# Optimization experiments

Measured on AMD Instinct MI355X. Metric: run time of the kernel, lower is better.

The kernel has to match this reference:

```python
import jax, jax.numpy as jnp
import numpy as np

SEQ_LEN = 2048
NUM_HEADS = 16
DIM_EMB = 1024
DIM_HEAD = DIM_EMB // NUM_HEADS  # 64
DIM_K = DIM_EMB  # source scales by dim_k**-0.5 with dim_k defaulting to dim_emb
BASE = 10000
EPS = float(np.finfo(np.float32).eps)


def _rope_tables(seq_len, dim_head):
    idx = jnp.arange(seq_len, dtype=jnp.float32)
    scale = 1.0 / (BASE ** (jnp.arange(0, dim_head, 2, dtype=jnp.float32) / dim_head) + EPS)
    pos = jnp.outer(idx, scale)              # [S, dh/2]
    pos = jnp.concatenate([pos, pos], axis=-1)  # [S, dh]
    return jnp.cos(pos), jnp.sin(pos)


def _rotate_half(x):
    x1, x2 = x[..., : DIM_HEAD // 2], x[..., DIM_HEAD // 2 :]
    return jnp.concatenate([-x2, x1], axis=-1)


def _apply_rope(x, cos, sin):
    # x: [B, H, S, dh]; cos/sin: [S, dh]
    return x * cos[None, None] + _rotate_half(x) * sin[None, None]


def setup_inputs() -> dict:
    key = jax.random.key(0)
    k1, k2, k3 = jax.random.split(key, 3)
    x = jax.random.normal(k1, (2, SEQ_LEN, DIM_EMB), dtype=jnp.float32)
    Wqkv = jax.random.normal(k2, (DIM_EMB, 3 * DIM_EMB), dtype=jnp.float32) * 0.02
    Wout = jax.random.normal(k3, (DIM_EMB, DIM_EMB), dtype=jnp.float32) * 0.02
    return {"x": x, "Wqkv": Wqkv, "Wout": Wout}


def reference(x, Wqkv, Wout):
    B = x.shape[0]
    cos, sin = _rope_tables(SEQ_LEN, DIM_HEAD)
    qkv = x @ Wqkv  # [B, S, 3*E]
    q, k, v = jnp.split(qkv, 3, axis=-1)

    def to_heads(t):
        return t.reshape(B, SEQ_LEN, NUM_HEADS, DIM_HEAD).transpose(0, 2, 1, 3)

    q, k, v = to_heads(q), to_heads(k), to_heads(v)
    q = _apply_rope(q, cos, sin)
    k = _apply_rope(k, cos, sin)

    scores = jnp.einsum('bhsd,bhtd->bhst', q, k) * (DIM_K ** -0.5)
    causal_mask = jnp.triu(jnp.ones((SEQ_LEN, SEQ_LEN), dtype=bool), k=1)
    scores = jnp.where(causal_mask[None, None], -jnp.inf, scores)
    attn = jax.nn.softmax(scores, axis=-1)
    out = jnp.einsum('bhst,bhtd->bhsd', attn, v)
    out = out.transpose(0, 2, 1, 3).reshape(B, SEQ_LEN, DIM_EMB)
    return out @ Wout
```

## Files before the change

kernel.cpp:

```cpp
#include <hip/hip_runtime.h>

#define S_LEN 2048
#define NHEAD 16

using f32x4  = __attribute__((ext_vector_type(4))) float;
using f32x16 = __attribute__((ext_vector_type(16))) float;
using bf16x8 = __attribute__((ext_vector_type(8))) __bf16;

__device__ __forceinline__ unsigned short f2bf(float f) {
  union { float f; unsigned u; } v; v.f = f;
  unsigned r = v.u + 0x7FFFu + ((v.u >> 16) & 1u);
  return (unsigned short)(r >> 16);
}
__device__ __forceinline__ float bf2f(unsigned short h) {
  union { unsigned u; float f; } v; v.u = ((unsigned)h) << 16; return v.f;
}
__device__ __forceinline__ void unpack8(uint4 u, float x[8]) {
  x[0]=bf2f((unsigned short)(u.x&0xffff)); x[1]=bf2f((unsigned short)(u.x>>16));
  x[2]=bf2f((unsigned short)(u.y&0xffff)); x[3]=bf2f((unsigned short)(u.y>>16));
  x[4]=bf2f((unsigned short)(u.z&0xffff)); x[5]=bf2f((unsigned short)(u.z>>16));
  x[6]=bf2f((unsigned short)(u.w&0xffff)); x[7]=bf2f((unsigned short)(u.w>>16));
}
__device__ __forceinline__ uint4 pack8(const unsigned short o[8]) {
  uint4 u;
  u.x = (unsigned)o[0] | ((unsigned)o[1]<<16);
  u.y = (unsigned)o[2] | ((unsigned)o[3]<<16);
  u.z = (unsigned)o[4] | ((unsigned)o[5]<<16);
  u.w = (unsigned)o[6] | ((unsigned)o[7]<<16);
  return u;
}
__device__ __forceinline__ void gload16(const void* g, void* l) {
  __builtin_amdgcn_global_load_lds(
      (const __attribute__((address_space(1))) unsigned int*)g,
      (__attribute__((address_space(3))) unsigned int*)l, 16, 0, 0);
}
__device__ __forceinline__ float exp2_fast(float x) {
#if __has_builtin(__builtin_amdgcn_exp2f)
  return __builtin_amdgcn_exp2f(x);
#else
  return __expf(x * 0.6931471805599453f);
#endif
}
__device__ __forceinline__ void store_c(float* C, size_t off, float v) { C[off] = v; }
__device__ __forceinline__ void store_c(unsigned short* C, size_t off, float v) { C[off] = f2bf(v); }

__global__ __launch_bounds__(256) void k_cvt(const float* __restrict__ in,
                                             unsigned short* __restrict__ out, int n8) {
  int i = blockIdx.x * 256 + threadIdx.x;
  if (i >= n8) return;
  const float4* p = (const float4*)in + 2 * (size_t)i;
  float4 a = p[0], b = p[1];
  unsigned short o[8] = { f2bf(a.x), f2bf(a.y), f2bf(a.z), f2bf(a.w),
                          f2bf(b.x), f2bf(b.y), f2bf(b.z), f2bf(b.w) };
  ((uint4*)out)[i] = pack8(o);
}

__global__ __launch_bounds__(256) void k_transpose_cvt(const float* __restrict__ in,
                                                       unsigned short* __restrict__ out,
                                                       int R, int C) {
  __shared__ float T[64][65];
  int r0 = blockIdx.x * 64, c0 = blockIdx.y * 64;
  int tid = threadIdx.x;
#pragma unroll
  for (int i = 0; i < 16; ++i) {
    int idx = tid + i * 256;
    int r = idx >> 6, c = idx & 63;
    T[r][c] = in[(size_t)(r0 + r) * C + c0 + c];
  }
  __syncthreads();
#pragma unroll
  for (int i = 0; i < 8; ++i) {
    int idx = tid + i * 256;
    int co = idx >> 5, rp = (idx & 31) * 2;
    unsigned v = (unsigned)f2bf(T[rp][co]) | ((unsigned)f2bf(T[rp + 1][co]) << 16);
    *(unsigned*)&out[(size_t)(c0 + co) * R + r0 + rp] = v;
  }
}

template <typename OUT_T>
__global__ __launch_bounds__(256, 2) void k_gemm128(const unsigned short* __restrict__ A,
                                                    const unsigned short* __restrict__ Bt,
                                                    OUT_T* __restrict__ C,
                                                    int M, int N, int K) {
  __shared__ unsigned short As[2][128][64];
  __shared__ unsigned short Bs[2][128][64];
  const int tid = threadIdx.x;
  const int lane = tid & 63, w = tid >> 6;
  const int wm = w >> 1, wn = w & 1;
  const int li = lane & 15, g = lane >> 4;
  const int m0 = blockIdx.x * 128, n0 = blockIdx.y * 128;
  const int srow = w * 8 + (lane >> 3);
  const int scol = ((lane & 7) ^ ((lane >> 3) & 7)) * 8;

  f32x4 acc[4][4];
#pragma unroll
  for (int i = 0; i < 4; ++i)
#pragma unroll
    for (int j = 0; j < 4; ++j) acc[i][j] = (f32x4){0.f, 0.f, 0.f, 0.f};

  const int nt = K >> 6;

  auto stage_tile = [&](int kt) {
    int buf = kt & 1;
    const unsigned short* sa = A + (size_t)(m0 + srow) * K + kt * 64 + scol;
    const unsigned short* sb = Bt + (size_t)(n0 + srow) * K + kt * 64 + scol;
    char* da = (char*)&As[buf][srow][0];
    char* db = (char*)&Bs[buf][srow][0];
#pragma unroll
    for (int j = 0; j < 4; ++j) {
      gload16(sa + (size_t)(j * 32) * K, da + j * 32 * 128);
      gload16(sb + (size_t)(j * 32) * K, db + j * 32 * 128);
    }
  };

  stage_tile(0);

  for (int i = 0; i < nt; ++i) {
    if (i + 1 < nt) {
      stage_tile(i + 1);
      asm volatile("s_waitcnt vmcnt(8)" ::: "memory");
    } else {
      asm volatile("s_waitcnt vmcnt(0)" ::: "memory");
    }
    __builtin_amdgcn_s_barrier();
    asm volatile("" ::: "memory");
    const int buf = i & 1;
#pragma unroll
    for (int kk = 0; kk < 2; ++kk) {
      bf16x8 af[4], bfv[4];
      const int ps = ((kk << 2) | g) ^ (li & 7);
#pragma unroll
      for (int ii = 0; ii < 4; ++ii)
        af[ii] = *(const bf16x8*)&As[buf][wm * 64 + ii * 16 + li][ps * 8];
#pragma unroll
      for (int jj = 0; jj < 4; ++jj)
        bfv[jj] = *(const bf16x8*)&Bs[buf][wn * 64 + jj * 16 + li][ps * 8];
      __builtin_amdgcn_s_setprio(1);
#pragma unroll
      for (int ii = 0; ii < 4; ++ii)
#pragma unroll
        for (int jj = 0; jj < 4; ++jj)
          acc[ii][jj] = __builtin_amdgcn_mfma_f32_16x16x32_bf16(af[ii], bfv[jj],
                                                                acc[ii][jj], 0, 0, 0);
      __builtin_amdgcn_s_setprio(0);
    }
    asm volatile("" ::: "memory");
    __builtin_amdgcn_s_barrier();
    asm volatile("" ::: "memory");
  }

#pragma unroll
  for (int ii = 0; ii < 4; ++ii) {
    int row = m0 + wm * 64 + ii * 16 + g * 4;
#pragma unroll
    for (int jj = 0; jj < 4; ++jj) {
      int col = n0 + wn * 64 + jj * 16 + li;
#pragma unroll
      for (int r = 0; r < 4; ++r) store_c(C, (size_t)(row + r) * N + col, acc[ii][jj][r]);
    }
  }
}

__global__ __launch_bounds__(256) void k_rope_split(const unsigned short* __restrict__ qkv,
                                                    unsigned short* __restrict__ Qf,
                                                    unsigned short* __restrict__ Kf,
                                                    unsigned short* __restrict__ Vf) {
  int blk = blockIdx.x;
  int st = blk & 31, h = (blk >> 5) & 15, b = blk >> 9;
  int s0 = st * 64;
  int tid = threadIdx.x;
  int sl = tid >> 2, quad = tid & 3;
  int s = s0 + sl;
  int bh = b * NHEAD + h;
  int l31 = s & 31;
  int qt = s >> 5;
  int cq = quad >> 1, hiq = quad & 1;

  float cs[8], sn[8];
#pragma unroll
  for (int j = 0; j < 8; ++j) {
    int pr = quad * 8 + j;
    float e2 = exp2_fast((float)pr * 0.41524101f);
    float freq = 1.0f / (e2 + 1.1920928955078125e-07f);
    float x = (float)s * freq * 0.15915494309189535f;
    x -= floorf(x);
    float ang = x * 6.283185307179586f;
    sn[j] = __sinf(ang);
    cs[j] = __cosf(ang);
  }
  const unsigned short* row = qkv + (size_t)(b * S_LEN + s) * 3072;
  const float QSC = 0.04508422f;
  {
    float x1[8], x2[8];
    unpack8(*(const uint4*)&row[h * 64 + quad * 8], x1);
    unpack8(*(const uint4*)&row[h * 64 + 32 + quad * 8], x2);
    unsigned short o1[8], o2[8];
#pragma unroll
    for (int j = 0; j < 8; ++j) {
      o1[j] = f2bf((x1[j] * cs[j] - x2[j] * sn[j]) * QSC);
      o2[j] = f2bf((x2[j] * cs[j] + x1[j] * sn[j]) * QSC);
    }
    size_t base = ((size_t)bh * 64 + qt) * 4;
    int lane8 = (hiq * 32 + l31) * 8;
    *(uint4*)&Qf[(base + cq) * 512 + lane8] = pack8(o1);
    *(uint4*)&Qf[(base + 2 + cq) * 512 + lane8] = pack8(o2);
  }
  {
    float x1[8], x2[8];
    unpack8(*(const uint4*)&row[1024 + h * 64 + quad * 8], x1);
    unpack8(*(const uint4*)&row[1024 + h * 64 + 32 + quad * 8], x2);
    unsigned short o1[8], o2[8];
#pragma unroll
    for (int j = 0; j < 8; ++j) {
      o1[j] = f2bf(x1[j] * cs[j] - x2[j] * sn[j]);
      o2[j] = f2bf(x2[j] * cs[j] + x1[j] * sn[j]);
    }
    int lp = (l31 & 0x13) | ((l31 & 4) << 1) | ((l31 & 8) >> 1);
    size_t base = ((size_t)bh * 64 + qt) * 4;
    int lane8 = (hiq * 32 + lp) * 8;
    *(uint4*)&Kf[(base + cq) * 512 + lane8] = pack8(o1);
    *(uint4*)&Kf[(base + 2 + cq) * 512 + lane8] = pack8(o2);
  }
  __shared__ unsigned short Vl[64 * 72];
#pragma unroll
  for (int i = 0; i < 2; ++i) {
    int c = tid + i * 256;
    int r = c >> 3, c8 = (c & 7) * 8;
    *(uint4*)&Vl[r * 72 + c8] =
        *(const uint4*)&qkv[(size_t)(b * S_LEN + s0 + r) * 3072 + 2048 + h * 64 + c8];
  }
  __syncthreads();
  int d = tid >> 2, sc4 = tid & 3;
  unsigned o[8];
#pragma unroll
  for (int jj = 0; jj < 8; ++jj) {
    int sidx = sc4 * 16 + jj * 2;
    o[jj] = (unsigned)Vl[sidx * 72 + d] | ((unsigned)Vl[(sidx + 1) * 72 + d] << 16);
  }
  {
    int t = st * 2 + (sc4 >> 1);
    int c = ((d >> 5) << 1) + (sc4 & 1);
    size_t base = (((size_t)bh * 64 + t) * 4 + c) * 512;
    *(uint4*)&Vf[base + (d & 31) * 8]        = make_uint4(o[0], o[1], o[2], o[3]);
    *(uint4*)&Vf[base + (32 + (d & 31)) * 8] = make_uint4(o[4], o[5], o[6], o[7]);
  }
}

__global__ __launch_bounds__(256) void k_attn5(const unsigned short* __restrict__ Qf,
                                               const unsigned short* __restrict__ Kf,
                                               const unsigned short* __restrict__ Vf,
                                               unsigned short* __restrict__ O) {
  __shared__ float MBUF[3][2176];
  int bid = blockIdx.x;
  int i = (bid & 7) * 256 + (bid >> 3);
  int bh = i >> 6;
  int qt = 63 - (i & 63);
  int tid = threadIdx.x, w = tid >> 6, lane = tid & 63;
  int b = bh >> 4, h = bh & 15;
  int l31 = lane & 31, hi = lane >> 5;

  int n = qt + 1;
  int t0 = (w * n) >> 2, t1 = ((w + 1) * n) >> 2;

  const unsigned short* Kg = Kf + ((size_t)bh * 64) * 4 * 512 + lane * 8;
  const unsigned short* Vg = Vf + ((size_t)bh * 64) * 4 * 512 + lane * 8;

  float m_run = -1e30f, l_run = 0.f;
  f32x16 acc0, acc1;
#pragma unroll
  for (int r = 0; r < 16; ++r) { acc0[r] = 0.f; acc1[r] = 0.f; }

  if (t0 < t1) {
    const unsigned short* Qg = Qf + (((size_t)bh * 64 + qt) * 4) * 512 + lane * 8;
    bf16x8 qf[4];
#pragma unroll
    for (int c = 0; c < 4; ++c) qf[c] = *(const bf16x8*)(Qg + c * 512);

    auto loadK = [&](bf16x8 (&kf)[4], int t) {
      const unsigned short* kp = Kg + (size_t)t * 2048;
#pragma unroll
      for (int c = 0; c < 4; ++c) kf[c] = *(const bf16x8*)(kp + c * 512);
    };
    auto loadV = [&](bf16x8 (&vf)[4], int t) {
      const unsigned short* vp = Vg + (size_t)t * 2048;
#pragma unroll
      for (int c = 0; c < 4; ++c) vf[c] = *(const bf16x8*)(vp + c * 512);
    };
    auto rescale_check = [&](float pmax) {
      if (__any(pmax > m_run + 8.0f)) {
        float pfull = fmaxf(pmax, __shfl_xor(pmax, 32));
        float mnew = fmaxf(m_run, pfull);
        float fac = exp2_fast(m_run - mnew);
        l_run *= fac;
#pragma unroll
        for (int r = 0; r < 16; ++r) { acc0[r] *= fac; acc1[r] *= fac; }
        m_run = mnew;
      }
    };
    auto cvt2 = [&](const f32x16& s, bf16x8& p0, bf16x8& p1) {
      unsigned w0, w1, w2, w3;
      asm("v_cvt_pk_bf16_f32 %0, %1, %2" : "=v"(w0) : "v"(s[0]), "v"(s[1]));
      asm("v_cvt_pk_bf16_f32 %0, %1, %2" : "=v"(w1) : "v"(s[2]), "v"(s[3]));
      asm("v_cvt_pk_bf16_f32 %0, %1, %2" : "=v"(w2) : "v"(s[4]), "v"(s[5]));
      asm("v_cvt_pk_bf16_f32 %0, %1, %2" : "=v"(w3) : "v"(s[6]), "v"(s[7]));
      union { uint4 uu; bf16x8 v; } cv;
      cv.uu = make_uint4(w0, w1, w2, w3);
      p0 = cv.v;
      asm("v_cvt_pk_bf16_f32 %0, %1, %2" : "=v"(w0) : "v"(s[8]), "v"(s[9]));
      asm("v_cvt_pk_bf16_f32 %0, %1, %2" : "=v"(w1) : "v"(s[10]), "v"(s[11]));
      asm("v_cvt_pk_bf16_f32 %0, %1, %2" : "=v"(w2) : "v"(s[12]), "v"(s[13]));
      asm("v_cvt_pk_bf16_f32 %0, %1, %2" : "=v"(w3) : "v"(s[14]), "v"(s[15]));
      cv.uu = make_uint4(w0, w1, w2, w3);
      p1 = cv.v;
    };

    bf16x8 kA[4], vA[4], kB[4], vB[4];
    loadK(kA, t0); loadV(vA, t0);
    if (t0 + 1 < t1) { loadK(kB, t0 + 1); loadV(vB, t0 + 1); }
    int t = t0;
    while (t + 1 < t1) {
      int tb = t + 1;
      f32x16 sa, sb;
#pragma unroll
      for (int r = 0; r < 16; ++r) { sa[r] = 0.f; sb[r] = 0.f; }
      __builtin_amdgcn_s_setprio(1);
      sa = __builtin_amdgcn_mfma_f32_32x32x16_bf16(kA[0], qf[0], sa, 0, 0, 0);
      sb = __builtin_amdgcn_mfma_f32_32x32x16_bf16(kB[0], qf[0], sb, 0, 0, 0);
      sa = __builtin_amdgcn_mfma_f32_32x32x16_bf16(kA[1], qf[1], sa, 0, 0, 0);
      sb = __builtin_amdgcn_mfma_f32_32x32x16_bf16(kB[1], qf[1], sb, 0, 0, 0);
      sa = __builtin_amdgcn_mfma_f32_32x32x16_bf16(kA[2], qf[2], sa, 0, 0, 0);
      sb = __builtin_amdgcn_mfma_f32_32x32x16_bf16(kB[2], qf[2], sb, 0, 0, 0);
      sa = __builtin_amdgcn_mfma_f32_32x32x16_bf16(kA[3], qf[3], sa, 0, 0, 0);
      sb = __builtin_amdgcn_mfma_f32_32x32x16_bf16(kB[3], qf[3], sb, 0, 0, 0);
      __builtin_amdgcn_s_setprio(0);
      if (t + 2 < t1) loadK(kA, t + 2);
      if (t + 3 < t1) loadK(kB, t + 3);
      if (tb == qt) {
#pragma unroll
        for (int r = 0; r < 16; ++r) {
          int kv = (r & 7) + 16 * (r >> 3) + 8 * hi;
          if (kv > l31) sb[r] = -1e30f;
        }
      }
      float pmax;
      {
        float m[8];
#pragma unroll
        for (int r = 0; r < 8; ++r)
          m[r] = fmaxf(fmaxf(sa[2 * r], sa[2 * r + 1]), fmaxf(sb[2 * r], sb[2 * r + 1]));
        m[0] = fmaxf(m[0], m[1]); m[2] = fmaxf(m[2], m[3]);
        m[4] = fmaxf(m[4], m[5]); m[6] = fmaxf(m[6], m[7]);
        pmax = fmaxf(fmaxf(m[0], m[2]), fmaxf(m[4], m[6]));
      }
      rescale_check(pmax);
#pragma unroll
      for (int r = 0; r < 16; ++r) {
        sa[r] = exp2_fast(sa[r] - m_run);
        sb[r] = exp2_fast(sb[r] - m_run);
      }
      {
        float t0_ = 0.f, t1_ = 0.f, t2_ = 0.f, t3_ = 0.f;
#pragma unroll
        for (int r = 0; r < 4; ++r) {
          t0_ += sa[r] + sb[r];
          t1_ += sa[4 + r] + sb[4 + r];
          t2_ += sa[8 + r] + sb[8 + r];
          t3_ += sa[12 + r] + sb[12 + r];
        }
        l_run += (t0_ + t1_) + (t2_ + t3_);
      }
      bf16x8 pa0, pa1, pb0, pb1;
      cvt2(sa, pa0, pa1);
      cvt2(sb, pb0, pb1);
      __builtin_amdgcn_s_setprio(1);
      acc0 = __builtin_amdgcn_mfma_f32_32x32x16_bf16(vA[0], pa0, acc0, 0, 0, 0);
      acc1 = __builtin_amdgcn_mfma_f32_32x32x16_bf16(vA[2], pa0, acc1, 0, 0, 0);
      acc0 = __builtin_amdgcn_mfma_f32_32x32x16_bf16(vA[1], pa1, acc0, 0, 0, 0);
      acc1 = __builtin_amdgcn_mfma_f32_32x32x16_bf16(vA[3], pa1, acc1, 0, 0, 0);
      acc0 = __builtin_amdgcn_mfma_f32_32x32x16_bf16(vB[0], pb0, acc0, 0, 0, 0);
      acc1 = __builtin_amdgcn_mfma_f32_32x32x16_bf16(vB[2], pb0, acc1, 0, 0, 0);
      acc0 = __builtin_amdgcn_mfma_f32_32x32x16_bf16(vB[1], pb1, acc0, 0, 0, 0);
      acc1 = __builtin_amdgcn_mfma_f32_32x32x16_bf16(vB[3], pb1, acc1, 0, 0, 0);
      __builtin_amdgcn_s_setprio(0);
      if (t + 2 < t1) loadV(vA, t + 2);
      if (t + 3 < t1) loadV(vB, t + 3);
      t += 2;
    }
    if (t < t1) {
      f32x16 s;
#pragma unroll
      for (int r = 0; r < 16; ++r) s[r] = 0.f;
      __builtin_amdgcn_s_setprio(1);
      s = __builtin_amdgcn_mfma_f32_32x32x16_bf16(kA[0], qf[0], s, 0, 0, 0);
      s = __builtin_amdgcn_mfma_f32_32x32x16_bf16(kA[1], qf[1], s, 0, 0, 0);
      s = __builtin_amdgcn_mfma_f32_32x32x16_bf16(kA[2], qf[2], s, 0, 0, 0);
      s = __builtin_amdgcn_mfma_f32_32x32x16_bf16(kA[3], qf[3], s, 0, 0, 0);
      __builtin_amdgcn_s_setprio(0);
      if (t == qt) {
#pragma unroll
        for (int r = 0; r < 16; ++r) {
          int kv = (r & 7) + 16 * (r >> 3) + 8 * hi;
          if (kv > l31) s[r] = -1e30f;
        }
      }
      float pmax;
      {
        float m0 = fmaxf(s[0], s[1]),   mm1 = fmaxf(s[2], s[3]);
        float m2 = fmaxf(s[4], s[5]),   m3 = fmaxf(s[6], s[7]);
        float m4 = fmaxf(s[8], s[9]),   m5 = fmaxf(s[10], s[11]);
        float m6 = fmaxf(s[12], s[13]), m7 = fmaxf(s[14], s[15]);
        m0 = fmaxf(m0, mm1); m2 = fmaxf(m2, m3); m4 = fmaxf(m4, m5); m6 = fmaxf(m6, m7);
        pmax = fmaxf(fmaxf(m0, m2), fmaxf(m4, m6));
      }
      rescale_check(pmax);
#pragma unroll
      for (int r = 0; r < 16; ++r) s[r] = exp2_fast(s[r] - m_run);
      {
        float s0 = (s[0] + s[1]) + (s[2] + s[3]);
        float s1 = (s[4] + s[5]) + (s[6] + s[7]);
        float s2 = (s[8] + s[9]) + (s[10] + s[11]);
        float s3 = (s[12] + s[13]) + (s[14] + s[15]);
        l_run += (s0 + s1) + (s2 + s3);
      }
      bf16x8 pf0, pf1;
      cvt2(s, pf0, pf1);
      __builtin_amdgcn_s_setprio(1);
      acc0 = __builtin_amdgcn_mfma_f32_32x32x16_bf16(vA[0], pf0, acc0, 0, 0, 0);
      acc0 = __builtin_amdgcn_mfma_f32_32x32x16_bf16(vA[1], pf1, acc0, 0, 0, 0);
      acc1 = __builtin_amdgcn_mfma_f32_32x32x16_bf16(vA[2], pf0, acc1, 0, 0, 0);
      acc1 = __builtin_amdgcn_mfma_f32_32x32x16_bf16(vA[3], pf1, acc1, 0, 0, 0);
      __builtin_amdgcn_s_setprio(0);
    }
  }

  if (w != 0) {
    float* sb = &MBUF[w - 1][0];
#pragma unroll
    for (int r = 0; r < 16; ++r) {
      sb[r * 64 + lane] = acc0[r];
      sb[(16 + r) * 64 + lane] = acc1[r];
    }
    sb[2048 + lane] = m_run;
    sb[2112 + lane] = l_run;
  }
  __syncthreads();
  if (w == 0) {
    float m1 = MBUF[0][2048 + lane], m2 = MBUF[1][2048 + lane], m3 = MBUF[2][2048 + lane];
    float mF = fmaxf(fmaxf(m_run, m1), fmaxf(m2, m3));
    float f0 = exp2_fast(m_run - mF);
    float f1 = exp2_fast(m1 - mF);
    float f2 = exp2_fast(m2 - mF);
    float f3 = exp2_fast(m3 - mF);
    float lF = f0 * l_run + f1 * MBUF[0][2112 + lane] + f2 * MBUF[1][2112 + lane] +
               f3 * MBUF[2][2112 + lane];
    lF += __shfl_xor(lF, 32);
    float inv = 1.0f / lF;
    f32x16 o0, o1;
#pragma unroll
    for (int r = 0; r < 16; ++r) {
      o0[r] = (f0 * acc0[r] + f1 * MBUF[0][r * 64 + lane] + f2 * MBUF[1][r * 64 + lane] +
               f3 * MBUF[2][r * 64 + lane]) * inv;
      o1[r] = (f0 * acc1[r] + f1 * MBUF[0][(16 + r) * 64 + lane] +
               f2 * MBUF[1][(16 + r) * 64 + lane] + f3 * MBUF[2][(16 + r) * 64 + lane]) * inv;
    }
    unsigned short* ol = (unsigned short*)&MBUF[0][0];
#pragma unroll
    for (int dh = 0; dh < 2; ++dh) {
#pragma unroll
      for (int r = 0; r < 16; r += 2) {
        int dv = dh * 32 + (r & 3) + 8 * (r >> 2) + 4 * hi;
        float lo = dh ? o1[r] : o0[r];
        float hi_ = dh ? o1[r + 1] : o0[r + 1];
        unsigned uu;
        asm("v_cvt_pk_bf16_f32 %0, %1, %2" : "=v"(uu) : "v"(lo), "v"(hi_));
        *(unsigned*)&ol[l31 * 72 + dv] = uu;
      }
    }
    asm volatile("s_waitcnt lgkmcnt(0)" ::: "memory");
    int q0f = qt * 32;
    int q = lane >> 1, half = lane & 1;
    unsigned short* op = O + ((size_t)(b * S_LEN + q0f + q)) * 1024 + h * 64 + half * 32;
#pragma unroll
    for (int j = 0; j < 4; ++j)
      *(uint4*)(op + j * 8) = *(const uint4*)&ol[q * 72 + half * 32 + j * 8];
  }
}

extern "C" void kernel_launch(void* const* d_in, const int* in_sizes, int n_in,
                              void* d_out, int out_size, void* d_ws, size_t ws_size,
                              hipStream_t stream) {
  const float* x = (const float*)d_in[0];
  const float* Wqkv = (const float*)d_in[1];
  const float* Wout = (const float*)d_in[2];
  float* out = (float*)d_out;
  char* ws = (char*)d_ws;
  unsigned short* xb = (unsigned short*)(ws);
  unsigned short* WqkvT = (unsigned short*)(ws + ((size_t)8 << 20));
  unsigned short* WoutT = (unsigned short*)(ws + ((size_t)14 << 20));
  unsigned short* qkv = (unsigned short*)(ws + ((size_t)16 << 20));
  unsigned short* Qf = (unsigned short*)(ws + ((size_t)40 << 20));
  unsigned short* Kf = (unsigned short*)(ws + ((size_t)48 << 20));
  unsigned short* Vf = (unsigned short*)(ws + ((size_t)56 << 20));

  k_cvt<<<2048, 256, 0, stream>>>(x, xb, 4096 * 1024 / 8);
  k_transpose_cvt<<<dim3(16, 48), 256, 0, stream>>>(Wqkv, WqkvT, 1024, 3072);
  k_transpose_cvt<<<dim3(16, 16), 256, 0, stream>>>(Wout, WoutT, 1024, 1024);
  k_gemm128<unsigned short><<<dim3(32, 24), 256, 0, stream>>>(xb, WqkvT, qkv, 4096, 3072, 1024);
  k_rope_split<<<1024, 256, 0, stream>>>(qkv, Qf, Kf, Vf);
  k_attn5<<<2048, 256, 0, stream>>>(Qf, Kf, Vf, xb );
  k_gemm128<float><<<dim3(32, 8), 256, 0, stream>>>(xb, WoutT, out, 4096, 1024, 1024);
}
```

Baseline: 120.2 us.

## Merge prep kernels into one launch and precompute RoPE trig table

Combines the x conversion and both weight transpose-conversions into a single k_prep launch, cutting two kernel launches. k_prep also adds extra blocks that build a cos/sin table per position, staged in the output buffer, which k_rope_split then reads in place of calling exp2/sin/cos itself. This removes launch overhead and repeated transcendental math. In exchange it adds a table write and read, and reuses the output buffer as scratch, which is safe only because the final GEMM overwrites it later.

```diff
diff --git a/kernel.cpp b/kernel.cpp
--- a/kernel.cpp
+++ b/kernel.cpp
@@ -44,23 +44,10 @@
 __device__ __forceinline__ void store_c(float* C, size_t off, float v) { C[off] = v; }
 __device__ __forceinline__ void store_c(unsigned short* C, size_t off, float v) { C[off] = f2bf(v); }
 
-__global__ __launch_bounds__(256) void k_cvt(const float* __restrict__ in,
-                                             unsigned short* __restrict__ out, int n8) {
-  int i = blockIdx.x * 256 + threadIdx.x;
-  if (i >= n8) return;
-  const float4* p = (const float4*)in + 2 * (size_t)i;
-  float4 a = p[0], b = p[1];
-  unsigned short o[8] = { f2bf(a.x), f2bf(a.y), f2bf(a.z), f2bf(a.w),
-                          f2bf(b.x), f2bf(b.y), f2bf(b.z), f2bf(b.w) };
-  ((uint4*)out)[i] = pack8(o);
-}
-
-__global__ __launch_bounds__(256) void k_transpose_cvt(const float* __restrict__ in,
-                                                       unsigned short* __restrict__ out,
-                                                       int R, int C) {
-  __shared__ float T[64][65];
-  int r0 = blockIdx.x * 64, c0 = blockIdx.y * 64;
-  int tid = threadIdx.x;
+__device__ __forceinline__ void transpose_body(const float* __restrict__ in,
+                                               unsigned short* __restrict__ out,
+                                               int R, int C, int r0, int c0,
+                                               float (*T)[65], int tid) {
 #pragma unroll
   for (int i = 0; i < 16; ++i) {
     int idx = tid + i * 256;
@@ -74,6 +61,45 @@
     int co = idx >> 5, rp = (idx & 31) * 2;
     unsigned v = (unsigned)f2bf(T[rp][co]) | ((unsigned)f2bf(T[rp + 1][co]) << 16);
     *(unsigned*)&out[(size_t)(c0 + co) * R + r0 + rp] = v;
+  }
+}
+
+__global__ __launch_bounds__(256) void k_prep(const float* __restrict__ x,
+                                              unsigned short* __restrict__ xb,
+                                              const float* __restrict__ Wqkv,
+                                              unsigned short* __restrict__ WqkvT,
+                                              const float* __restrict__ Wout,
+                                              unsigned short* __restrict__ WoutT,
+                                              float2* __restrict__ tab) {
+  __shared__ float T[64][65];
+  int blk = blockIdx.x;
+  int tid = threadIdx.x;
+  if (blk < 2048) {
+    int i = blk * 256 + tid;
+    const float4* p = (const float4*)x + 2 * (size_t)i;
+    float4 a = p[0], b = p[1];
+    unsigned short o[8] = { f2bf(a.x), f2bf(a.y), f2bf(a.z), f2bf(a.w),
+                            f2bf(b.x), f2bf(b.y), f2bf(b.z), f2bf(b.w) };
+    ((uint4*)xb)[i] = pack8(o);
+  } else if (blk < 2816) {
+    int b2 = blk - 2048;
+    transpose_body(Wqkv, WqkvT, 1024, 3072, (b2 & 15) * 64, (b2 >> 4) * 64, T, tid);
+  } else if (blk < 3072) {
+    int b3 = blk - 2816;
+    transpose_body(Wout, WoutT, 1024, 1024, (b3 & 15) * 64, (b3 >> 4) * 64, T, tid);
+  } else {
+    int gt = (blk - 3072) * 256 + tid;
+    int s = gt >> 2, quad = gt & 3;
+#pragma unroll
+    for (int j = 0; j < 8; ++j) {
+      int pr = quad * 8 + j;
+      float e2 = exp2_fast((float)pr * 0.41524101f);
+      float freq = 1.0f / (e2 + 1.1920928955078125e-07f);
+      float xx = (float)s * freq * 0.15915494309189535f;
+      xx -= floorf(xx);
+      float ang = xx * 6.283185307179586f;
+      tab[(size_t)s * 32 + pr] = make_float2(__cosf(ang), __sinf(ang));
+    }
   }
 }
 
@@ -162,6 +188,7 @@
 }
 
 __global__ __launch_bounds__(256) void k_rope_split(const unsigned short* __restrict__ qkv,
+                                                    const float2* __restrict__ tab,
                                                     unsigned short* __restrict__ Qf,
                                                     unsigned short* __restrict__ Kf,
                                                     unsigned short* __restrict__ Vf) {
@@ -177,16 +204,10 @@
   int cq = quad >> 1, hiq = quad & 1;
 
   float cs[8], sn[8];
-#pragma unroll
-  for (int j = 0; j < 8; ++j) {
-    int pr = quad * 8 + j;
-    float e2 = exp2_fast((float)pr * 0.41524101f);
-    float freq = 1.0f / (e2 + 1.1920928955078125e-07f);
-    float x = (float)s * freq * 0.15915494309189535f;
-    x -= floorf(x);
-    float ang = x * 6.283185307179586f;
-    sn[j] = __sinf(ang);
-    cs[j] = __cosf(ang);
+  {
+    const float2* tp = tab + (size_t)s * 32 + quad * 8;
+#pragma unroll
+    for (int j = 0; j < 8; ++j) { float2 t = tp[j]; cs[j] = t.x; sn[j] = t.y; }
   }
   const unsigned short* row = qkv + (size_t)(b * S_LEN + s) * 3072;
   const float QSC = 0.04508422f;
@@ -501,12 +522,11 @@
   unsigned short* Qf = (unsigned short*)(ws + ((size_t)40 << 20));
   unsigned short* Kf = (unsigned short*)(ws + ((size_t)48 << 20));
   unsigned short* Vf = (unsigned short*)(ws + ((size_t)56 << 20));
-
-  k_cvt<<<2048, 256, 0, stream>>>(x, xb, 4096 * 1024 / 8);
-  k_transpose_cvt<<<dim3(16, 48), 256, 0, stream>>>(Wqkv, WqkvT, 1024, 3072);
-  k_transpose_cvt<<<dim3(16, 16), 256, 0, stream>>>(Wout, WoutT, 1024, 1024);
+  float2* trig = (float2*)d_out;
+
+  k_prep<<<3104, 256, 0, stream>>>(x, xb, Wqkv, WqkvT, Wout, WoutT, trig);
   k_gemm128<unsigned short><<<dim3(32, 24), 256, 0, stream>>>(xb, WqkvT, qkv, 4096, 3072, 1024);
-  k_rope_split<<<1024, 256, 0, stream>>>(qkv, Qf, Kf, Vf);
+  k_rope_split<<<1024, 256, 0, stream>>>(qkv, trig, Qf, Kf, Vf);
   k_attn5<<<2048, 256, 0, stream>>>(Qf, Kf, Vf, xb );
   k_gemm128<float><<<dim3(32, 8), 256, 0, stream>>>(xb, WoutT, out, 4096, 1024, 1024);
 }
```

Result: faster. 116.4 us, median of 2 (-3.2%).
